# Kernel tuning notes

Hardware: AMD Instinct MI355X
Metric: run time of the kernel (lower is better)

Reference implementation:

```python
import jax, jax.numpy as jnp
import numpy as np

DIM = 256
NUM_HEADS = 4
HEAD_DIM = DIM // NUM_HEADS
EPS = 1e-5


def setup_inputs() -> dict:
    key = jax.random.key(0)
    ks = jax.random.split(key, 8)
    B, N, C = 8, 2048, DIM
    s = 0.02
    return {
        "x": jax.random.normal(ks[0], (B, N, C), jnp.float32),
        "qkv_w": jax.random.normal(ks[1], (C, 3 * C), jnp.float32) * s,
        "qkv_b": jnp.zeros((3 * C,), jnp.float32),
        "proj_w": jax.random.normal(ks[2], (C, C), jnp.float32) * s,
        "proj_b": jnp.zeros((C,), jnp.float32),
        "ln1_g": jnp.ones((C,), jnp.float32),
        "ln1_b": jnp.zeros((C,), jnp.float32),
        "ln2_g": jnp.ones((C,), jnp.float32),
        "ln2_b": jnp.zeros((C,), jnp.float32),
        "mlp_w1": jax.random.normal(ks[3], (C, 2 * C), jnp.float32) * s,
        "mlp_b1": jnp.zeros((2 * C,), jnp.float32),
        "mlp_w2": jax.random.normal(ks[4], (2 * C, C), jnp.float32) * s,
        "mlp_b2": jnp.zeros((C,), jnp.float32),
    }


def _layernorm(x, g, b):
    mu = jnp.mean(x, axis=-1, keepdims=True)
    var = jnp.mean(jnp.square(x - mu), axis=-1, keepdims=True)
    return (x - mu) * jax.lax.rsqrt(var + EPS) * g + b


def reference(x, qkv_w, qkv_b, proj_w, proj_b, ln1_g, ln1_b, ln2_g, ln2_b,
              mlp_w1, mlp_b1, mlp_w2, mlp_b2):
    B, N, C = x.shape
    H, D = NUM_HEADS, HEAD_DIM
    shortcut = x
    h = _layernorm(x, ln1_g, ln1_b)
    qkv = (h @ qkv_w + qkv_b).reshape(B, N, 3, H, D)
    q = qkv[:, :, 0].transpose(0, 2, 1, 3)  # [B,H,N,D]
    k = qkv[:, :, 1].transpose(0, 2, 1, 3)
    v = qkv[:, :, 2].transpose(0, 2, 1, 3)
    attn = jnp.einsum('bhnd,bhmd->bhnm', q, k) * (D ** -0.5)
    attn = jax.nn.softmax(attn, axis=-1)  # dropout = identity (eval mode)
    o = jnp.einsum('bhnm,bhmd->bhnd', attn, v)
    o = o.transpose(0, 2, 1, 3).reshape(B, N, C)
    x = o @ proj_w + proj_b + shortcut
    h2 = _layernorm(x, ln2_g, ln2_b)
    mlp = jax.nn.gelu(h2 @ mlp_w1 + mlp_b1, approximate=False) @ mlp_w2 + mlp_b2
    return x + mlp
```

## Files before the change

kernel.cpp:

```cpp
#include <hip/hip_runtime.h>

typedef __bf16 bf16;
typedef __bf16 bf16x8 __attribute__((ext_vector_type(8)));
typedef __bf16 bf16x4 __attribute__((ext_vector_type(4)));
typedef float  f32x4  __attribute__((ext_vector_type(4)));
typedef unsigned u32x2 __attribute__((ext_vector_type(2)));

typedef __attribute__((address_space(1))) const void GASV;
typedef __attribute__((address_space(3))) void LASV;

__device__ __forceinline__ void gload16(const void* g, void* l) {
  __builtin_amdgcn_global_load_lds((GASV*)g, (LASV*)l, 16, 0, 0);
}

constexpr float CEXP = 0.125f * 1.44269504088896340736f;

__global__ __launch_bounds__(256) void wconv_all(const float* __restrict__ qkv_w,
                                                 const float* __restrict__ proj_w,
                                                 const float* __restrict__ w1,
                                                 const float* __restrict__ w2,
                                                 bf16* __restrict__ Wtqkv,
                                                 bf16* __restrict__ WtP,
                                                 bf16* __restrict__ Wt1,
                                                 bf16* __restrict__ Wt2) {
  __shared__ float td[32][33];
  const int t = blockIdx.x;
  const float* src;
  bf16* dst;
  int Kin, Nin, kt, nt;
  if (t < 192)      { src = qkv_w; dst = Wtqkv; Kin = 256; Nin = 768; kt = t & 7;          nt = t >> 3; }
  else if (t < 256) { src = proj_w; dst = WtP;  Kin = 256; Nin = 256; kt = (t - 192) & 7;  nt = (t - 192) >> 3; }
  else if (t < 384) { src = w1;    dst = Wt1;   Kin = 256; Nin = 512; kt = (t - 256) & 7;  nt = (t - 256) >> 3; }
  else              { src = w2;    dst = Wt2;   Kin = 512; Nin = 256; kt = (t - 384) & 15; nt = (t - 384) >> 4; }
  const int tid = threadIdx.x;
  {
    const int r = tid >> 3, c4 = (tid & 7) << 2;
    const float4 v = *(const float4*)(src + (size_t)(kt * 32 + r) * Nin + nt * 32 + c4);
    td[r][c4 + 0] = v.x; td[r][c4 + 1] = v.y; td[r][c4 + 2] = v.z; td[r][c4 + 3] = v.w;
  }
  __syncthreads();
  {
    const int n = tid >> 3, k4 = (tid & 7) << 2;
    bf16x4 o;
#pragma unroll
    for (int i = 0; i < 4; ++i) o[i] = (bf16)td[k4 + i][n];
    *(bf16x4*)(dst + (size_t)(nt * 32 + n) * Kin + kt * 32 + k4) = o;
  }
}

__global__ __launch_bounds__(256) void ln_fwd(const float* __restrict__ x,
                                              const float* __restrict__ gam,
                                              const float* __restrict__ bet,
                                              bf16* __restrict__ out) {
  const int lane = threadIdx.x & 63;
  const int w = threadIdx.x >> 6;
  const size_t row = (size_t)blockIdx.x * 4 + w;
  const float4 v = *(const float4*)(x + row * 256 + lane * 4);
  float s1 = v.x + v.y + v.z + v.w;
  float s2 = v.x * v.x + v.y * v.y + v.z * v.z + v.w * v.w;
#pragma unroll
  for (int m = 1; m < 64; m <<= 1) {
    s1 += __shfl_xor(s1, m);
    s2 += __shfl_xor(s2, m);
  }
  const float mu = s1 * (1.0f / 256.0f);
  const float var = s2 * (1.0f / 256.0f) - mu * mu;
  const float rs = rsqrtf(var + 1e-5f);
  const float4 g4 = *(const float4*)(gam + lane * 4);
  const float4 b4 = *(const float4*)(bet + lane * 4);
  bf16x4 o;
  o[0] = (bf16)((v.x - mu) * rs * g4.x + b4.x);
  o[1] = (bf16)((v.y - mu) * rs * g4.y + b4.y);
  o[2] = (bf16)((v.z - mu) * rs * g4.z + b4.z);
  o[3] = (bf16)((v.w - mu) * rs * g4.w + b4.w);
  *(bf16x4*)(out + row * 256 + lane * 4) = o;
}

template <int EPI>
__global__ __launch_bounds__(256) void gemm64(const bf16* __restrict__ A,
                                              const bf16* __restrict__ Bt,
                                              const float* __restrict__ bias,
                                              const float* __restrict__ res,
                                              void* __restrict__ outp,
                                              int M, int N, int K) {
  __shared__ bf16 Al[2][4096];
  __shared__ bf16 Bl[2][4096];
  const int tid = threadIdx.x;
  const int lane = tid & 63;
  const int W = tid >> 6;
  const int wm = W >> 1, wn = W & 1;
  const int nbm = M >> 6;
  const int bm = (int)blockIdx.x % nbm;
  const int bn = (int)blockIdx.x / nbm;
  const int m0 = bm << 6, n0 = bn << 6;
  const int nk = K >> 6;

  const char* asrc[2];
  const char* bsrc[2];
#pragma unroll
  for (int p = 0; p < 2; ++p) {
    const int s = W + 4 * p;
    const int row = (s >> 2) * 32 + (((s >> 1) & 1) << 4) + (lane & 15);
    const int kb = (((s & 1) << 5) + ((lane >> 4) << 3)) * 2;
    asrc[p] = (const char*)(A + (size_t)(m0 + row) * K) + kb;
    bsrc[p] = (const char*)(Bt + (size_t)(n0 + row) * K) + kb;
  }

  auto stage = [&](int sl) {
    char* ad = (char*)&Al[sl][0] + W * 1024;
    char* bd = (char*)&Bl[sl][0] + W * 1024;
    gload16(asrc[0], ad);
    gload16(asrc[1], ad + 4096);
    gload16(bsrc[0], bd);
    gload16(bsrc[1], bd + 4096);
    asrc[0] += 128; asrc[1] += 128; bsrc[0] += 128; bsrc[1] += 128;
  };

  f32x4 acc[2][2];
#pragma unroll
  for (int i = 0; i < 2; ++i)
#pragma unroll
    for (int j = 0; j < 2; ++j) acc[i][j] = (f32x4){0.f, 0.f, 0.f, 0.f};

  stage(0);
  asm volatile("s_waitcnt vmcnt(0)" ::: "memory");
  __builtin_amdgcn_s_barrier();

  for (int t = 0; t < nk; ++t) {
    if (t + 1 < nk) stage((t + 1) & 1);
    const char* pa = (const char*)&Al[t & 1][0] + wm * 4096 + lane * 16;
    const char* pb = (const char*)&Bl[t & 1][0] + wn * 4096 + lane * 16;
    bf16x8 av[2][2], bv[2][2];
#pragma unroll
    for (int f = 0; f < 2; ++f)
#pragma unroll
      for (int ks = 0; ks < 2; ++ks) {
        av[f][ks] = *(const bf16x8*)(pa + (f * 2 + ks) * 1024);
        bv[f][ks] = *(const bf16x8*)(pb + (f * 2 + ks) * 1024);
      }
    __builtin_amdgcn_s_setprio(1);
#pragma unroll
    for (int fm = 0; fm < 2; ++fm)
#pragma unroll
      for (int fn = 0; fn < 2; ++fn) {
        acc[fm][fn] = __builtin_amdgcn_mfma_f32_16x16x32_bf16(av[fm][0], bv[fn][0], acc[fm][fn], 0, 0, 0);
        acc[fm][fn] = __builtin_amdgcn_mfma_f32_16x16x32_bf16(av[fm][1], bv[fn][1], acc[fm][fn], 0, 0, 0);
      }
    __builtin_amdgcn_s_setprio(0);
    asm volatile("s_waitcnt vmcnt(0)" ::: "memory");
    __builtin_amdgcn_s_barrier();
  }

#pragma unroll
  for (int fm = 0; fm < 2; ++fm)
#pragma unroll
    for (int fn = 0; fn < 2; ++fn) {
      const int r0 = m0 + wm * 32 + fm * 16 + ((lane >> 4) << 2);
      const int c = n0 + wn * 32 + fn * 16 + (lane & 15);
#pragma unroll
      for (int j = 0; j < 4; ++j) {
        const int r = r0 + j;
        const float v = acc[fm][fn][j];
        if constexpr (EPI == 0) {
          ((bf16*)outp)[(size_t)r * N + c] = (bf16)(v + bias[c]);
        } else if constexpr (EPI == 1) {
          ((bf16*)outp)[(size_t)r * 2048 + ((size_t)(c >> 11)) * 524288 + (c & 2047)] =
              (bf16)(v + bias[r]);
        } else if constexpr (EPI == 2) {
          ((float*)outp)[(size_t)r * N + c] = v + bias[c] + res[(size_t)r * N + c];
        } else {
          const float u = v + bias[c];
          ((bf16*)outp)[(size_t)r * N + c] = (bf16)(u * 0.5f * (1.0f + erff(u * 0.70710678118f)));
        }
      }
    }
}

__global__ __launch_bounds__(256) void attn_fwd(const bf16* __restrict__ qk,
                                                const bf16* __restrict__ vT,
                                                bf16* __restrict__ po,
                                                float* __restrict__ pstats) {
  __shared__ bf16 Kl[2][4096];
  __shared__ bf16 Vl[2][4096];
  __shared__ bf16 Pl[4][1024];
  const int tid = threadIdx.x;
  const int lane = tid & 63;
  const int w = tid >> 6;
  const int g = lane >> 4;
  const int qi = lane & 15;
  const int bid = (int)blockIdx.x;
  const int bh = bid & 31;
  const int qt = (bid >> 5) & 15;
  const int s = bid >> 9;
  const int b = bh >> 2, h = bh & 3;

  const size_t qrow0 = (size_t)b * 2048 + qt * 128 + w * 32 + qi;
  bf16x8 qf[2][2];
#pragma unroll
  for (int f = 0; f < 2; ++f) {
    const bf16* qp = qk + (qrow0 + f * 16) * 512 + h * 64 + g * 8;
    qf[f][0] = *(const bf16x8*)qp;
    qf[f][1] = *(const bf16x8*)(qp + 32);
  }

  float mrun[2] = {0.f, 0.f};
  float lsum[2] = {0.f, 0.f};
  f32x4 o[4][2];
#pragma unroll
  for (int i = 0; i < 4; ++i)
#pragma unroll
    for (int f = 0; f < 2; ++f) o[i][f] = (f32x4){0.f, 0.f, 0.f, 0.f};

  constexpr float THR = 8.0f / CEXP;

  const char* kbase = (const char*)qk + ((size_t)b * 2048) * 1024 + 512 + h * 128 +
                      (size_t)s * 16 * 65536;
  const char* vbase = (const char*)vT + (size_t)bh * 262144 + (size_t)s * 16 * 128;
  const char* ks[2];
  const char* vs[2];
#pragma unroll
  for (int i = 0; i < 2; ++i) {
    const int fk = i * 2 + (w >> 1);
    const int half = w & 1;
    ks[i] = kbase + (fk * 16 + qi) * 1024 + half * 64 + g * 16;
    vs[i] = vbase + (size_t)(fk * 16 + qi) * 4096 + half * 64 + g * 16;
  }
  char* const pw = (char*)&Pl[w][0];
  int paddrb[2];
#pragma unroll
  for (int bb = 0; bb < 2; ++bb)
    paddrb[bb] = (bb * 2 + (g >> 1)) * 256 + qi * 16 + (g & 1) * 8;
  const char* const prd = pw + lane * 16;

  auto stage = [&](int slot) {
    char* kd = (char*)&Kl[0][0] + slot * 8192 + w * 1024;
    char* vd = (char*)&Vl[0][0] + slot * 8192 + w * 1024;
    gload16(ks[0], kd);
    gload16(ks[1], kd + 4096);
    gload16(vs[0], vd);
    gload16(vs[1], vd + 4096);
    ks[0] += 65536; ks[1] += 65536;
    vs[0] += 128;   vs[1] += 128;
  };

  stage(0);
  asm volatile("s_waitcnt vmcnt(0)" ::: "memory");
  __builtin_amdgcn_s_barrier();

  for (int t = 0; t < 16; ++t) {
    if (t < 15) stage((t + 1) & 1);
    const char* kb = (const char*)&Kl[0][0] + (t & 1) * 8192 + lane * 16;
    f32x4 st[4][2];
    __builtin_amdgcn_s_setprio(1);
#pragma unroll
    for (int fk = 0; fk < 4; ++fk) {
      const bf16x8 k0 = *(const bf16x8*)(kb + fk * 2048);
      const bf16x8 k1 = *(const bf16x8*)(kb + fk * 2048 + 1024);
#pragma unroll
      for (int f = 0; f < 2; ++f) {
        f32x4 z = (f32x4){0.f, 0.f, 0.f, 0.f};
        st[fk][f] = __builtin_amdgcn_mfma_f32_16x16x32_bf16(k0, qf[f][0], z, 0, 0, 0);
        st[fk][f] = __builtin_amdgcn_mfma_f32_16x16x32_bf16(k1, qf[f][1], st[fk][f], 0, 0, 0);
      }
    }
    __builtin_amdgcn_s_setprio(0);
    float pmax[2];
#pragma unroll
    for (int f = 0; f < 2; ++f) {
      float m0 = fmaxf(fmaxf(st[0][f][0], st[0][f][1]), fmaxf(st[0][f][2], st[0][f][3]));
      float m1 = fmaxf(fmaxf(st[1][f][0], st[1][f][1]), fmaxf(st[1][f][2], st[1][f][3]));
      float m2 = fmaxf(fmaxf(st[2][f][0], st[2][f][1]), fmaxf(st[2][f][2], st[2][f][3]));
      float m3 = fmaxf(fmaxf(st[3][f][0], st[3][f][1]), fmaxf(st[3][f][2], st[3][f][3]));
      pmax[f] = fmaxf(fmaxf(m0, m1), fmaxf(m2, m3));
    }
    if (!__all(pmax[0] <= mrun[0] + THR && pmax[1] <= mrun[1] + THR)) {
#pragma unroll
      for (int f = 0; f < 2; ++f) {
        float mt = fmaxf(pmax[f], __shfl_xor(pmax[f], 16));
        mt = fmaxf(mt, __shfl_xor(mt, 32));
        const float mnew = fmaxf(mrun[f], mt);
        const float alpha = exp2f(CEXP * (mrun[f] - mnew));
        lsum[f] *= alpha;
#pragma unroll
        for (int fd = 0; fd < 4; ++fd)
#pragma unroll
          for (int j = 0; j < 4; ++j) o[fd][f][j] *= alpha;
        mrun[f] = mnew;
      }
    }
    unsigned pk[4][2][2];
#pragma unroll
    for (int f = 0; f < 2; ++f) {
      const float negcm = -CEXP * mrun[f];
      float ts = 0.f;
#pragma unroll
      for (int fk = 0; fk < 4; ++fk)
#pragma unroll
        for (int jp = 0; jp < 2; ++jp) {
          const float p0 = exp2f(fmaf(st[fk][f][2 * jp], CEXP, negcm));
          const float p1 = exp2f(fmaf(st[fk][f][2 * jp + 1], CEXP, negcm));
          ts += p0 + p1;
          union { bf16 h2[2]; unsigned u; } cv;
          cv.h2[0] = (bf16)p0;
          cv.h2[1] = (bf16)p1;
          pk[fk][f][jp] = cv.u;
        }
      lsum[f] += ts;
    }
    const char* vb = (const char*)&Vl[0][0] + (t & 1) * 8192 + lane * 16;
#pragma unroll
    for (int ksl = 0; ksl < 2; ++ksl) {
#pragma unroll
      for (int bb = 0; bb < 2; ++bb) {
        const int fk = 2 * ksl + bb;
#pragma unroll
        for (int f = 0; f < 2; ++f) {
          u32x2 pv2;
          pv2[0] = pk[fk][f][0];
          pv2[1] = pk[fk][f][1];
          *(u32x2*)(pw + f * 1024 + paddrb[bb]) = pv2;
        }
      }
      bf16x8 pa[2];
#pragma unroll
      for (int f = 0; f < 2; ++f) pa[f] = *(const bf16x8*)(prd + f * 1024);
      __builtin_amdgcn_s_setprio(1);
#pragma unroll
      for (int fd = 0; fd < 4; ++fd) {
        const bf16x8 vv = *(const bf16x8*)(vb + fd * 2048 + ksl * 1024);
#pragma unroll
        for (int f = 0; f < 2; ++f)
          o[fd][f] = __builtin_amdgcn_mfma_f32_16x16x32_bf16(vv, pa[f], o[fd][f], 0, 0, 0);
      }
      __builtin_amdgcn_s_setprio(0);
    }
    asm volatile("s_waitcnt vmcnt(0)" ::: "memory");
    __builtin_amdgcn_s_barrier();
  }

#pragma unroll
  for (int f = 0; f < 2; ++f) {
    float l = lsum[f];
    l += __shfl_xor(l, 16);
    l += __shfl_xor(l, 32);
    lsum[f] = l;
  }
  if (g == 0) {
#pragma unroll
    for (int f = 0; f < 2; ++f) {
      float2 sv;
      sv.x = mrun[f];
      sv.y = lsum[f];
      *(float2*)(pstats + (((size_t)s * 32 + bh) * 2048 + qt * 128 + w * 32 + f * 16 + qi) * 2) = sv;
    }
  }
#pragma unroll
  for (int f = 0; f < 2; ++f) {
    bf16* const orow = po + ((size_t)s * 16384 + qrow0 + f * 16) * 256 + h * 64 + g * 4;
#pragma unroll
    for (int fd = 0; fd < 4; ++fd) {
      bf16x4 ov;
#pragma unroll
      for (int j = 0; j < 4; ++j) ov[j] = (bf16)o[fd][f][j];
      *(bf16x4*)(orow + fd * 16) = ov;
    }
  }
}

__global__ __launch_bounds__(256) void attn_merge(const bf16* __restrict__ po,
                                                  const float* __restrict__ pstats,
                                                  bf16* __restrict__ ob) {
  const int idx = blockIdx.x * 256 + threadIdx.x;
  const int r = idx >> 6;
  const int cq = (idx & 63) * 4;
  const int h = cq >> 6;
  const int bh = (r >> 11) * 4 + h;
  const int ql = r & 2047;
  const float2 s0 = *(const float2*)(pstats + (((size_t)bh) * 2048 + ql) * 2);
  const float2 s1 = *(const float2*)(pstats + (((size_t)32 + bh) * 2048 + ql) * 2);
  const float M = fmaxf(s0.x, s1.x);
  const float a0 = exp2f(CEXP * (s0.x - M));
  const float a1 = exp2f(CEXP * (s1.x - M));
  const float inv = 1.0f / (s0.y * a0 + s1.y * a1);
  const bf16x4 p0 = *(const bf16x4*)(po + (size_t)r * 256 + cq);
  const bf16x4 p1 = *(const bf16x4*)(po + ((size_t)16384 + r) * 256 + cq);
  bf16x4 ov;
#pragma unroll
  for (int j = 0; j < 4; ++j)
    ov[j] = (bf16)(((float)p0[j] * a0 + (float)p1[j] * a1) * inv);
  *(bf16x4*)(ob + (size_t)r * 256 + cq) = ov;
}

extern "C" void kernel_launch(void* const* d_in, const int* in_sizes, int n_in,
                              void* d_out, int out_size, void* d_ws, size_t ws_size,
                              hipStream_t stream) {
  const float* x      = (const float*)d_in[0];
  const float* qkv_w  = (const float*)d_in[1];
  const float* qkv_b  = (const float*)d_in[2];
  const float* proj_w = (const float*)d_in[3];
  const float* proj_b = (const float*)d_in[4];
  const float* ln1_g  = (const float*)d_in[5];
  const float* ln1_b  = (const float*)d_in[6];
  const float* ln2_g  = (const float*)d_in[7];
  const float* ln2_b  = (const float*)d_in[8];
  const float* mlp_w1 = (const float*)d_in[9];
  const float* mlp_b1 = (const float*)d_in[10];
  const float* mlp_w2 = (const float*)d_in[11];
  const float* mlp_b2 = (const float*)d_in[12];
  float* out = (float*)d_out;

  char* ws = (char*)d_ws;
  bf16* Wtqkv = (bf16*)(ws);
  bf16* WtP   = (bf16*)(ws + 393216);
  bf16* Wt1   = (bf16*)(ws + 524288);
  bf16* Wt2   = (bf16*)(ws + 786432);
  bf16* h     = (bf16*)(ws + 1048576);
  bf16* qkb   = (bf16*)(ws + 9437184);
  bf16* vT    = (bf16*)(ws + 26214400);
  bf16* obuf  = (bf16*)(ws + 34603008);
  float* x2   = (float*)(ws + 42991616);
  bf16* po    = (bf16*)(ws + 42991616);
  float* pstats = (float*)(ws + 59768832);
  bf16* a1 = qkb;
  bf16* h2 = h;

  wconv_all<<<512, 256, 0, stream>>>(qkv_w, proj_w, mlp_w1, mlp_w2, Wtqkv, WtP, Wt1, Wt2);

  ln_fwd<<<4096, 256, 0, stream>>>(x, ln1_g, ln1_b, h);
  gemm64<0><<<2048, 256, 0, stream>>>(h, Wtqkv, qkv_b, nullptr, qkb, 16384, 512, 256);
  gemm64<1><<<1024, 256, 0, stream>>>(Wtqkv + 512 * 256, h, qkv_b + 512, nullptr, vT, 256, 16384, 256);
  attn_fwd<<<1024, 256, 0, stream>>>(qkb, vT, po, pstats);
  attn_merge<<<4096, 256, 0, stream>>>(po, pstats, obuf);
  gemm64<2><<<1024, 256, 0, stream>>>(obuf, WtP, proj_b, x, x2, 16384, 256, 256);
  ln_fwd<<<4096, 256, 0, stream>>>(x2, ln2_g, ln2_b, h2);
  gemm64<3><<<2048, 256, 0, stream>>>(h2, Wt1, mlp_b1, nullptr, a1, 16384, 512, 256);
  gemm64<2><<<1024, 256, 0, stream>>>(a1, Wt2, mlp_b2, x2, out, 16384, 256, 512);
}
```

Measured before the change: 194.0 us.

## Enlarge GEMM tiles to 128x128 and fuse attention split-merge into projection GEMM

GEMM tiles grow from 64x64 to 128x128, so each wave now computes a 4x4 block of MFMA fragments. This raises register and LDS use and reduces the number of blocks to 256-512, which may underfill the 256 CUs. The separate attn_merge kernel is removed; the projection GEMM instead loads both partial attention outputs and their softmax stats and combines them while staging the A tile into LDS. The two partial outputs are also placed in separate buffers, one of them reusing the LN buffer, which saves a kernel launch and a full round-trip of the merged activation.

Result: faster. 178.2 us (-8.1%).

```diff
diff --git a/kernel.cpp b/kernel.cpp
--- a/kernel.cpp
+++ b/kernel.cpp
@@ -77,62 +77,110 @@
 }
 
 template <int EPI>
-__global__ __launch_bounds__(256) void gemm64(const bf16* __restrict__ A,
-                                              const bf16* __restrict__ Bt,
-                                              const float* __restrict__ bias,
-                                              const float* __restrict__ res,
-                                              void* __restrict__ outp,
-                                              int M, int N, int K) {
-  __shared__ bf16 Al[2][4096];
-  __shared__ bf16 Bl[2][4096];
+__global__ __launch_bounds__(256) void gemm_bt(const bf16* __restrict__ A,
+                                               const bf16* __restrict__ Bt,
+                                               const float* __restrict__ bias,
+                                               const float* __restrict__ res,
+                                               void* __restrict__ outp,
+                                               int M, int N, int K,
+                                               const bf16* __restrict__ A2,
+                                               const float* __restrict__ pstats) {
+  constexpr bool MA = (EPI == 4);
+  __shared__ bf16 Al[2][8192];
+  __shared__ bf16 Bl[2][8192];
   const int tid = threadIdx.x;
   const int lane = tid & 63;
   const int W = tid >> 6;
   const int wm = W >> 1, wn = W & 1;
-  const int nbm = M >> 6;
+  const int qi = lane & 15, g = lane >> 4;
+  const int nbm = M >> 7;
   const int bm = (int)blockIdx.x % nbm;
   const int bn = (int)blockIdx.x / nbm;
-  const int m0 = bm << 6, n0 = bn << 6;
+  const int m0 = bm << 7, n0 = bn << 7;
   const int nk = K >> 6;
 
-  const char* asrc[2];
-  const char* bsrc[2];
-#pragma unroll
-  for (int p = 0; p < 2; ++p) {
-    const int s = W + 4 * p;
-    const int row = (s >> 2) * 32 + (((s >> 1) & 1) << 4) + (lane & 15);
-    const int kb = (((s & 1) << 5) + ((lane >> 4) << 3)) * 2;
+  int rowg[4];
+  const char* asrc[4];
+  const char* bsrc[4];
+#pragma unroll
+  for (int p = 0; p < 4; ++p) {
+    const int s = W * 4 + p;
+    const int row = (s >> 3) * 64 + ((s >> 1) & 3) * 16 + qi;
+    const int kb = (s & 1) * 64 + g * 16;
+    rowg[p] = m0 + row;
     asrc[p] = (const char*)(A + (size_t)(m0 + row) * K) + kb;
     bsrc[p] = (const char*)(Bt + (size_t)(n0 + row) * K) + kb;
   }
 
-  auto stage = [&](int sl) {
-    char* ad = (char*)&Al[sl][0] + W * 1024;
-    char* bd = (char*)&Bl[sl][0] + W * 1024;
-    gload16(asrc[0], ad);
-    gload16(asrc[1], ad + 4096);
-    gload16(bsrc[0], bd);
-    gload16(bsrc[1], bd + 4096);
-    asrc[0] += 128; asrc[1] += 128; bsrc[0] += 128; bsrc[1] += 128;
+  f32x4 acc[4][4];
+#pragma unroll
+  for (int i = 0; i < 4; ++i)
+#pragma unroll
+    for (int j = 0; j < 4; ++j) acc[i][j] = (f32x4){0.f, 0.f, 0.f, 0.f};
+
+  bf16x8 pa0v[4], pa1v[4];
+  float2 sst0[4], sst1[4];
+
+  auto stagePlain = [&](int sl) {
+#pragma unroll
+    for (int p = 0; p < 4; ++p) {
+      gload16(asrc[p], (char*)&Al[sl][0] + (W * 4 + p) * 1024);
+      gload16(bsrc[p], (char*)&Bl[sl][0] + (W * 4 + p) * 1024);
+      asrc[p] += 128;
+      bsrc[p] += 128;
+    }
   };
-
-  f32x4 acc[2][2];
-#pragma unroll
-  for (int i = 0; i < 2; ++i)
-#pragma unroll
-    for (int j = 0; j < 2; ++j) acc[i][j] = (f32x4){0.f, 0.f, 0.f, 0.f};
-
-  stage(0);
+  auto stageMAload = [&](int sl, int t) {
+#pragma unroll
+    for (int p = 0; p < 4; ++p) {
+      gload16(bsrc[p], (char*)&Bl[sl][0] + (W * 4 + p) * 1024);
+      bsrc[p] += 128;
+      pa0v[p] = *(const bf16x8*)(asrc[p]);
+      pa1v[p] = *(const bf16x8*)((const char*)A2 + (asrc[p] - (const char*)A));
+      asrc[p] += 128;
+      const int bh = ((rowg[p] >> 11) << 2) + t;
+      const int ql = rowg[p] & 2047;
+      sst0[p] = *(const float2*)(pstats + ((size_t)bh * 2048 + ql) * 2);
+      sst1[p] = *(const float2*)(pstats + ((size_t)(bh + 32) * 2048 + ql) * 2);
+    }
+  };
+  auto stageMAwrite = [&](int sl) {
+#pragma unroll
+    for (int p = 0; p < 4; ++p) {
+      const float mx = fmaxf(sst0[p].x, sst1[p].x);
+      float a0 = exp2f(CEXP * (sst0[p].x - mx));
+      float a1 = exp2f(CEXP * (sst1[p].x - mx));
+      const float inv = 1.0f / (sst0[p].y * a0 + sst1[p].y * a1);
+      a0 *= inv;
+      a1 *= inv;
+      bf16x8 wv;
+#pragma unroll
+      for (int j = 0; j < 8; ++j)
+        wv[j] = (bf16)((float)pa0v[p][j] * a0 + (float)pa1v[p][j] * a1);
+      *(bf16x8*)((char*)&Al[sl][0] + (W * 4 + p) * 1024 + lane * 16) = wv;
+    }
+  };
+
+  if constexpr (MA) {
+    stageMAload(0, 0);
+    stageMAwrite(0);
+  } else {
+    stagePlain(0);
+  }
   asm volatile("s_waitcnt vmcnt(0)" ::: "memory");
+  if constexpr (MA) asm volatile("s_waitcnt lgkmcnt(0)" ::: "memory");
   __builtin_amdgcn_s_barrier();
 
   for (int t = 0; t < nk; ++t) {
-    if (t + 1 < nk) stage((t + 1) & 1);
-    const char* pa = (const char*)&Al[t & 1][0] + wm * 4096 + lane * 16;
-    const char* pb = (const char*)&Bl[t & 1][0] + wn * 4096 + lane * 16;
-    bf16x8 av[2][2], bv[2][2];
-#pragma unroll
-    for (int f = 0; f < 2; ++f)
+    if (t + 1 < nk) {
+      if constexpr (MA) stageMAload((t + 1) & 1, t + 1);
+      else stagePlain((t + 1) & 1);
+    }
+    const char* pa = (const char*)&Al[t & 1][0] + wm * 8192 + lane * 16;
+    const char* pb = (const char*)&Bl[t & 1][0] + wn * 8192 + lane * 16;
+    bf16x8 av[4][2], bv[4][2];
+#pragma unroll
+    for (int f = 0; f < 4; ++f)
 #pragma unroll
       for (int ks = 0; ks < 2; ++ks) {
         av[f][ks] = *(const bf16x8*)(pa + (f * 2 + ks) * 1024);
@@ -140,23 +188,27 @@
       }
     __builtin_amdgcn_s_setprio(1);
 #pragma unroll
-    for (int fm = 0; fm < 2; ++fm)
-#pragma unroll
-      for (int fn = 0; fn < 2; ++fn) {
+    for (int fm = 0; fm < 4; ++fm)
+#pragma unroll
+      for (int fn = 0; fn < 4; ++fn) {
         acc[fm][fn] = __builtin_amdgcn_mfma_f32_16x16x32_bf16(av[fm][0], bv[fn][0], acc[fm][fn], 0, 0, 0);
         acc[fm][fn] = __builtin_amdgcn_mfma_f32_16x16x32_bf16(av[fm][1], bv[fn][1], acc[fm][fn], 0, 0, 0);
       }
     __builtin_amdgcn_s_setprio(0);
+    if (t + 1 < nk) {
+      if constexpr (MA) stageMAwrite((t + 1) & 1);
+    }
     asm volatile("s_waitcnt vmcnt(0)" ::: "memory");
+    if constexpr (MA) asm volatile("s_waitcnt lgkmcnt(0)" ::: "memory");
     __builtin_amdgcn_s_barrier();
   }
 
 #pragma unroll
-  for (int fm = 0; fm < 2; ++fm)
-#pragma unroll
-    for (int fn = 0; fn < 2; ++fn) {
-      const int r0 = m0 + wm * 32 + fm * 16 + ((lane >> 4) << 2);
-      const int c = n0 + wn * 32 + fn * 16 + (lane & 15);
+  for (int fm = 0; fm < 4; ++fm)
+#pragma unroll
+    for (int fn = 0; fn < 4; ++fn) {
+      const int r0 = m0 + wm * 64 + fm * 16 + ((lane >> 4) << 2);
+      const int c = n0 + wn * 64 + fn * 16 + (lane & 15);
 #pragma unroll
       for (int j = 0; j < 4; ++j) {
         const int r = r0 + j;
@@ -166,7 +218,7 @@
         } else if constexpr (EPI == 1) {
           ((bf16*)outp)[(size_t)r * 2048 + ((size_t)(c >> 11)) * 524288 + (c & 2047)] =
               (bf16)(v + bias[r]);
-        } else if constexpr (EPI == 2) {
+        } else if constexpr (EPI == 2 || EPI == 4) {
           ((float*)outp)[(size_t)r * N + c] = v + bias[c] + res[(size_t)r * N + c];
         } else {
           const float u = v + bias[c];
@@ -178,7 +230,8 @@
 
 __global__ __launch_bounds__(256) void attn_fwd(const bf16* __restrict__ qk,
                                                 const bf16* __restrict__ vT,
-                                                bf16* __restrict__ po,
+                                                bf16* __restrict__ po0,
+                                                bf16* __restrict__ po1,
                                                 float* __restrict__ pstats) {
   __shared__ bf16 Kl[2][4096];
   __shared__ bf16 Vl[2][4096];
@@ -354,9 +407,10 @@
       *(float2*)(pstats + (((size_t)s * 32 + bh) * 2048 + qt * 128 + w * 32 + f * 16 + qi) * 2) = sv;
     }
   }
+  bf16* const pob = s ? po1 : po0;
 #pragma unroll
   for (int f = 0; f < 2; ++f) {
-    bf16* const orow = po + ((size_t)s * 16384 + qrow0 + f * 16) * 256 + h * 64 + g * 4;
+    bf16* const orow = pob + (qrow0 + f * 16) * 256 + h * 64 + g * 4;
 #pragma unroll
     for (int fd = 0; fd < 4; ++fd) {
       bf16x4 ov;
@@ -365,30 +419,6 @@
       *(bf16x4*)(orow + fd * 16) = ov;
     }
   }
-}
-
-__global__ __launch_bounds__(256) void attn_merge(const bf16* __restrict__ po,
-                                                  const float* __restrict__ pstats,
-                                                  bf16* __restrict__ ob) {
-  const int idx = blockIdx.x * 256 + threadIdx.x;
-  const int r = idx >> 6;
-  const int cq = (idx & 63) * 4;
-  const int h = cq >> 6;
-  const int bh = (r >> 11) * 4 + h;
-  const int ql = r & 2047;
-  const float2 s0 = *(const float2*)(pstats + (((size_t)bh) * 2048 + ql) * 2);
-  const float2 s1 = *(const float2*)(pstats + (((size_t)32 + bh) * 2048 + ql) * 2);
-  const float M = fmaxf(s0.x, s1.x);
-  const float a0 = exp2f(CEXP * (s0.x - M));
-  const float a1 = exp2f(CEXP * (s1.x - M));
-  const float inv = 1.0f / (s0.y * a0 + s1.y * a1);
-  const bf16x4 p0 = *(const bf16x4*)(po + (size_t)r * 256 + cq);
-  const bf16x4 p1 = *(const bf16x4*)(po + ((size_t)16384 + r) * 256 + cq);
-  bf16x4 ov;
-#pragma unroll
-  for (int j = 0; j < 4; ++j)
-    ov[j] = (bf16)(((float)p0[j] * a0 + (float)p1[j] * a1) * inv);
-  *(bf16x4*)(ob + (size_t)r * 256 + cq) = ov;
 }
 
 extern "C" void kernel_launch(void* const* d_in, const int* in_sizes, int n_in,
@@ -417,22 +447,21 @@
   bf16* h     = (bf16*)(ws + 1048576);
   bf16* qkb   = (bf16*)(ws + 9437184);
   bf16* vT    = (bf16*)(ws + 26214400);
-  bf16* obuf  = (bf16*)(ws + 34603008);
+  bf16* po1   = (bf16*)(ws + 34603008);
   float* x2   = (float*)(ws + 42991616);
-  bf16* po    = (bf16*)(ws + 42991616);
   float* pstats = (float*)(ws + 59768832);
+  bf16* po0 = h;
   bf16* a1 = qkb;
   bf16* h2 = h;
 
   wconv_all<<<512, 256, 0, stream>>>(qkv_w, proj_w, mlp_w1, mlp_w2, Wtqkv, WtP, Wt1, Wt2);
 
   ln_fwd<<<4096, 256, 0, stream>>>(x, ln1_g, ln1_b, h);
-  gemm64<0><<<2048, 256, 0, stream>>>(h, Wtqkv, qkv_b, nullptr, qkb, 16384, 512, 256);
-  gemm64<1><<<1024, 256, 0, stream>>>(Wtqkv + 512 * 256, h, qkv_b + 512, nullptr, vT, 256, 16384, 256);
-  attn_fwd<<<1024, 256, 0, stream>>>(qkb, vT, po, pstats);
-  attn_merge<<<4096, 256, 0, stream>>>(po, pstats, obuf);
-  gemm64<2><<<1024, 256, 0, stream>>>(obuf, WtP, proj_b, x, x2, 16384, 256, 256);
+  gemm_bt<0><<<512, 256, 0, stream>>>(h, Wtqkv, qkv_b, nullptr, qkb, 16384, 512, 256, nullptr, nullptr);
+  gemm_bt<1><<<256, 256, 0, stream>>>(Wtqkv + 512 * 256, h, qkv_b + 512, nullptr, vT, 256, 16384, 256, nullptr, nullptr);
+  attn_fwd<<<1024, 256, 0, stream>>>(qkb, vT, po0, po1, pstats);
+  gemm_bt<4><<<256, 256, 0, stream>>>(po0, WtP, proj_b, x, x2, 16384, 256, 256, po1, pstats);
   ln_fwd<<<4096, 256, 0, stream>>>(x2, ln2_g, ln2_b, h2);
-  gemm64<3><<<2048, 256, 0, stream>>>(h2, Wt1, mlp_b1, nullptr, a1, 16384, 512, 256);
-  gemm64<2><<<1024, 256, 0, stream>>>(a1, Wt2, mlp_b2, x2, out, 16384, 256, 512);
-}
+  gemm_bt<3><<<512, 256, 0, stream>>>(h2, Wt1, mlp_b1, nullptr, a1, 16384, 512, 256, nullptr, nullptr);
+  gemm_bt<2><<<256, 256, 0, stream>>>(a1, Wt2, mlp_b2, x2, out, 16384, 256, 512, nullptr, nullptr);
+}
```

## Enlarge GEMM tiles to 128x128 with 8 waves and fuse LN1 into weight prep

Applied to the files above, without the earlier changes.

The GEMM kernel moves from 64x64 tiles with 4 waves to 128x128 tiles with 8 waves per block, each wave computing 64x32. This doubles operand reuse from LDS and quarters the block count. The first layernorm is folded into the weight-conversion launch, saving one kernel launch. Attention partial outputs are split into two buffers that alias the no-longer-live h and vT regions, so the workspace layout changes. The trade-off is fewer blocks (256–512) for the GPU to fill, plus larger LDS and register use per block.

New measurement: 170.7 us. -12.0%, faster.

```diff
diff --git a/kernel.cpp b/kernel.cpp
--- a/kernel.cpp
+++ b/kernel.cpp
@@ -15,16 +15,47 @@
 
 constexpr float CEXP = 0.125f * 1.44269504088896340736f;
 
-__global__ __launch_bounds__(256) void wconv_all(const float* __restrict__ qkv_w,
-                                                 const float* __restrict__ proj_w,
-                                                 const float* __restrict__ w1,
-                                                 const float* __restrict__ w2,
-                                                 bf16* __restrict__ Wtqkv,
-                                                 bf16* __restrict__ WtP,
-                                                 bf16* __restrict__ Wt1,
-                                                 bf16* __restrict__ Wt2) {
+__global__ __launch_bounds__(256) void prep_fused(const float* __restrict__ qkv_w,
+                                                  const float* __restrict__ proj_w,
+                                                  const float* __restrict__ w1,
+                                                  const float* __restrict__ w2,
+                                                  bf16* __restrict__ Wtqkv,
+                                                  bf16* __restrict__ WtP,
+                                                  bf16* __restrict__ Wt1,
+                                                  bf16* __restrict__ Wt2,
+                                                  const float* __restrict__ x,
+                                                  const float* __restrict__ gam,
+                                                  const float* __restrict__ bet,
+                                                  bf16* __restrict__ hout) {
   __shared__ float td[32][33];
-  const int t = blockIdx.x;
+  const int blk = blockIdx.x;
+  const int tid = threadIdx.x;
+  if (blk >= 512) {
+    const int lane = tid & 63;
+    const int w = tid >> 6;
+    const size_t row = (size_t)(blk - 512) * 4 + w;
+    const float4 v = *(const float4*)(x + row * 256 + lane * 4);
+    float s1 = v.x + v.y + v.z + v.w;
+    float s2 = v.x * v.x + v.y * v.y + v.z * v.z + v.w * v.w;
+#pragma unroll
+    for (int m = 1; m < 64; m <<= 1) {
+      s1 += __shfl_xor(s1, m);
+      s2 += __shfl_xor(s2, m);
+    }
+    const float mu = s1 * (1.0f / 256.0f);
+    const float var = s2 * (1.0f / 256.0f) - mu * mu;
+    const float rs = rsqrtf(var + 1e-5f);
+    const float4 g4 = *(const float4*)(gam + lane * 4);
+    const float4 b4 = *(const float4*)(bet + lane * 4);
+    bf16x4 o;
+    o[0] = (bf16)((v.x - mu) * rs * g4.x + b4.x);
+    o[1] = (bf16)((v.y - mu) * rs * g4.y + b4.y);
+    o[2] = (bf16)((v.z - mu) * rs * g4.z + b4.z);
+    o[3] = (bf16)((v.w - mu) * rs * g4.w + b4.w);
+    *(bf16x4*)(hout + row * 256 + lane * 4) = o;
+    return;
+  }
+  const int t = blk;
   const float* src;
   bf16* dst;
   int Kin, Nin, kt, nt;
@@ -32,7 +63,6 @@
   else if (t < 256) { src = proj_w; dst = WtP;  Kin = 256; Nin = 256; kt = (t - 192) & 7;  nt = (t - 192) >> 3; }
   else if (t < 384) { src = w1;    dst = Wt1;   Kin = 256; Nin = 512; kt = (t - 256) & 7;  nt = (t - 256) >> 3; }
   else              { src = w2;    dst = Wt2;   Kin = 512; Nin = 256; kt = (t - 384) & 15; nt = (t - 384) >> 4; }
-  const int tid = threadIdx.x;
   {
     const int r = tid >> 3, c4 = (tid & 7) << 2;
     const float4 v = *(const float4*)(src + (size_t)(kt * 32 + r) * Nin + nt * 32 + c4);
@@ -77,50 +107,51 @@
 }
 
 template <int EPI>
-__global__ __launch_bounds__(256) void gemm64(const bf16* __restrict__ A,
-                                              const bf16* __restrict__ Bt,
-                                              const float* __restrict__ bias,
-                                              const float* __restrict__ res,
-                                              void* __restrict__ outp,
-                                              int M, int N, int K) {
-  __shared__ bf16 Al[2][4096];
-  __shared__ bf16 Bl[2][4096];
+__global__ __launch_bounds__(512) void gemm_bt(const bf16* __restrict__ A,
+                                               const bf16* __restrict__ Bt,
+                                               const float* __restrict__ bias,
+                                               const float* __restrict__ res,
+                                               void* __restrict__ outp,
+                                               int M, int N, int K) {
+  __shared__ bf16 Al[2][8192];
+  __shared__ bf16 Bl[2][8192];
   const int tid = threadIdx.x;
   const int lane = tid & 63;
   const int W = tid >> 6;
-  const int wm = W >> 1, wn = W & 1;
-  const int nbm = M >> 6;
+  const int wm = W >> 2, wn = W & 3;
+  const int qi = lane & 15, g = lane >> 4;
+  const int nbm = M >> 7;
   const int bm = (int)blockIdx.x % nbm;
   const int bn = (int)blockIdx.x / nbm;
-  const int m0 = bm << 6, n0 = bn << 6;
+  const int m0 = bm << 7, n0 = bn << 7;
   const int nk = K >> 6;
 
   const char* asrc[2];
   const char* bsrc[2];
 #pragma unroll
   for (int p = 0; p < 2; ++p) {
-    const int s = W + 4 * p;
-    const int row = (s >> 2) * 32 + (((s >> 1) & 1) << 4) + (lane & 15);
-    const int kb = (((s & 1) << 5) + ((lane >> 4) << 3)) * 2;
+    const int s = p * 8 + W;
+    const int row = (s >> 3) * 64 + ((s >> 1) & 3) * 16 + qi;
+    const int kb = (s & 1) * 64 + g * 16;
     asrc[p] = (const char*)(A + (size_t)(m0 + row) * K) + kb;
     bsrc[p] = (const char*)(Bt + (size_t)(n0 + row) * K) + kb;
   }
 
+  f32x4 acc[4][2];
+#pragma unroll
+  for (int i = 0; i < 4; ++i)
+#pragma unroll
+    for (int j = 0; j < 2; ++j) acc[i][j] = (f32x4){0.f, 0.f, 0.f, 0.f};
+
   auto stage = [&](int sl) {
-    char* ad = (char*)&Al[sl][0] + W * 1024;
-    char* bd = (char*)&Bl[sl][0] + W * 1024;
-    gload16(asrc[0], ad);
-    gload16(asrc[1], ad + 4096);
-    gload16(bsrc[0], bd);
-    gload16(bsrc[1], bd + 4096);
-    asrc[0] += 128; asrc[1] += 128; bsrc[0] += 128; bsrc[1] += 128;
+#pragma unroll
+    for (int p = 0; p < 2; ++p) {
+      gload16(asrc[p], (char*)&Al[sl][0] + (p * 8 + W) * 1024);
+      gload16(bsrc[p], (char*)&Bl[sl][0] + (p * 8 + W) * 1024);
+      asrc[p] += 128;
+      bsrc[p] += 128;
+    }
   };
-
-  f32x4 acc[2][2];
-#pragma unroll
-  for (int i = 0; i < 2; ++i)
-#pragma unroll
-    for (int j = 0; j < 2; ++j) acc[i][j] = (f32x4){0.f, 0.f, 0.f, 0.f};
 
   stage(0);
   asm volatile("s_waitcnt vmcnt(0)" ::: "memory");
@@ -128,19 +159,24 @@
 
   for (int t = 0; t < nk; ++t) {
     if (t + 1 < nk) stage((t + 1) & 1);
-    const char* pa = (const char*)&Al[t & 1][0] + wm * 4096 + lane * 16;
-    const char* pb = (const char*)&Bl[t & 1][0] + wn * 4096 + lane * 16;
-    bf16x8 av[2][2], bv[2][2];
-#pragma unroll
-    for (int f = 0; f < 2; ++f)
+    const char* pa = (const char*)&Al[t & 1][0] + wm * 8192 + lane * 16;
+    const char* pb = (const char*)&Bl[t & 1][0] + lane * 16;
+    bf16x8 av[4][2], bv[2][2];
+#pragma unroll
+    for (int f = 0; f < 4; ++f)
+#pragma unroll
+      for (int ks = 0; ks < 2; ++ks)
+        av[f][ks] = *(const bf16x8*)(pa + (f * 2 + ks) * 1024);
+#pragma unroll
+    for (int fn = 0; fn < 2; ++fn)
 #pragma unroll
       for (int ks = 0; ks < 2; ++ks) {
-        av[f][ks] = *(const bf16x8*)(pa + (f * 2 + ks) * 1024);
-        bv[f][ks] = *(const bf16x8*)(pb + (f * 2 + ks) * 1024);
+        const int r16 = wn * 2 + fn;
+        bv[fn][ks] = *(const bf16x8*)(pb + ((r16 >> 2) * 8 + (r16 & 3) * 2 + ks) * 1024);
       }
     __builtin_amdgcn_s_setprio(1);
 #pragma unroll
-    for (int fm = 0; fm < 2; ++fm)
+    for (int fm = 0; fm < 4; ++fm)
 #pragma unroll
       for (int fn = 0; fn < 2; ++fn) {
         acc[fm][fn] = __builtin_amdgcn_mfma_f32_16x16x32_bf16(av[fm][0], bv[fn][0], acc[fm][fn], 0, 0, 0);
@@ -152,11 +188,11 @@
   }
 
 #pragma unroll
-  for (int fm = 0; fm < 2; ++fm)
+  for (int fm = 0; fm < 4; ++fm)
 #pragma unroll
     for (int fn = 0; fn < 2; ++fn) {
-      const int r0 = m0 + wm * 32 + fm * 16 + ((lane >> 4) << 2);
-      const int c = n0 + wn * 32 + fn * 16 + (lane & 15);
+      const int r0 = m0 + wm * 64 + fm * 16 + g * 4;
+      const int c = n0 + wn * 32 + fn * 16 + qi;
 #pragma unroll
       for (int j = 0; j < 4; ++j) {
         const int r = r0 + j;
@@ -178,7 +214,8 @@
 
 __global__ __launch_bounds__(256) void attn_fwd(const bf16* __restrict__ qk,
                                                 const bf16* __restrict__ vT,
-                                                bf16* __restrict__ po,
+                                                bf16* __restrict__ po0,
+                                                bf16* __restrict__ po1,
                                                 float* __restrict__ pstats) {
   __shared__ bf16 Kl[2][4096];
   __shared__ bf16 Vl[2][4096];
@@ -354,9 +391,10 @@
       *(float2*)(pstats + (((size_t)s * 32 + bh) * 2048 + qt * 128 + w * 32 + f * 16 + qi) * 2) = sv;
     }
   }
+  bf16* const pob = s ? po1 : po0;
 #pragma unroll
   for (int f = 0; f < 2; ++f) {
-    bf16* const orow = po + ((size_t)s * 16384 + qrow0 + f * 16) * 256 + h * 64 + g * 4;
+    bf16* const orow = pob + (qrow0 + f * 16) * 256 + h * 64 + g * 4;
 #pragma unroll
     for (int fd = 0; fd < 4; ++fd) {
       bf16x4 ov;
@@ -367,7 +405,8 @@
   }
 }
 
-__global__ __launch_bounds__(256) void attn_merge(const bf16* __restrict__ po,
+__global__ __launch_bounds__(256) void attn_merge(const bf16* __restrict__ po0,
+                                                  const bf16* __restrict__ po1,
                                                   const float* __restrict__ pstats,
                                                   bf16* __restrict__ ob) {
   const int idx = blockIdx.x * 256 + threadIdx.x;
@@ -382,8 +421,8 @@
   const float a0 = exp2f(CEXP * (s0.x - M));
   const float a1 = exp2f(CEXP * (s1.x - M));
   const float inv = 1.0f / (s0.y * a0 + s1.y * a1);
-  const bf16x4 p0 = *(const bf16x4*)(po + (size_t)r * 256 + cq);
-  const bf16x4 p1 = *(const bf16x4*)(po + ((size_t)16384 + r) * 256 + cq);
+  const bf16x4 p0 = *(const bf16x4*)(po0 + (size_t)r * 256 + cq);
+  const bf16x4 p1 = *(const bf16x4*)(po1 + (size_t)r * 256 + cq);
   bf16x4 ov;
 #pragma unroll
   for (int j = 0; j < 4; ++j)
@@ -417,22 +456,22 @@
   bf16* h     = (bf16*)(ws + 1048576);
   bf16* qkb   = (bf16*)(ws + 9437184);
   bf16* vT    = (bf16*)(ws + 26214400);
-  bf16* obuf  = (bf16*)(ws + 34603008);
+  bf16* po1   = (bf16*)(ws + 34603008);
   float* x2   = (float*)(ws + 42991616);
-  bf16* po    = (bf16*)(ws + 42991616);
   float* pstats = (float*)(ws + 59768832);
+  bf16* po0  = h;
+  bf16* obuf = vT;
   bf16* a1 = qkb;
   bf16* h2 = h;
 
-  wconv_all<<<512, 256, 0, stream>>>(qkv_w, proj_w, mlp_w1, mlp_w2, Wtqkv, WtP, Wt1, Wt2);
-
-  ln_fwd<<<4096, 256, 0, stream>>>(x, ln1_g, ln1_b, h);
-  gemm64<0><<<2048, 256, 0, stream>>>(h, Wtqkv, qkv_b, nullptr, qkb, 16384, 512, 256);
-  gemm64<1><<<1024, 256, 0, stream>>>(Wtqkv + 512 * 256, h, qkv_b + 512, nullptr, vT, 256, 16384, 256);
-  attn_fwd<<<1024, 256, 0, stream>>>(qkb, vT, po, pstats);
-  attn_merge<<<4096, 256, 0, stream>>>(po, pstats, obuf);
-  gemm64<2><<<1024, 256, 0, stream>>>(obuf, WtP, proj_b, x, x2, 16384, 256, 256);
+  prep_fused<<<4608, 256, 0, stream>>>(qkv_w, proj_w, mlp_w1, mlp_w2, Wtqkv, WtP, Wt1, Wt2,
+                                       x, ln1_g, ln1_b, h);
+  gemm_bt<0><<<512, 512, 0, stream>>>(h, Wtqkv, qkv_b, nullptr, qkb, 16384, 512, 256);
+  gemm_bt<1><<<256, 512, 0, stream>>>(Wtqkv + 512 * 256, h, qkv_b + 512, nullptr, vT, 256, 16384, 256);
+  attn_fwd<<<1024, 256, 0, stream>>>(qkb, vT, po0, po1, pstats);
+  attn_merge<<<4096, 256, 0, stream>>>(po0, po1, pstats, obuf);
+  gemm_bt<2><<<256, 512, 0, stream>>>(obuf, WtP, proj_b, x, x2, 16384, 256, 256);
   ln_fwd<<<4096, 256, 0, stream>>>(x2, ln2_g, ln2_b, h2);
-  gemm64<3><<<2048, 256, 0, stream>>>(h2, Wt1, mlp_b1, nullptr, a1, 16384, 512, 256);
-  gemm64<2><<<1024, 256, 0, stream>>>(a1, Wt2, mlp_b2, x2, out, 16384, 256, 512);
-}
+  gemm_bt<3><<<512, 512, 0, stream>>>(h2, Wt1, mlp_b1, nullptr, a1, 16384, 512, 256);
+  gemm_bt<2><<<256, 512, 0, stream>>>(a1, Wt2, mlp_b2, x2, out, 16384, 256, 512);
+}
```
